# Optimization experiments

Hardware: AMD Instinct MI355X
Metric: run time of the kernel (lower is better)

## Reference

```python
import jax, jax.numpy as jnp
import numpy as np

L = 32      # num_layer
N_ORD = 64  # order_of_a_LTImodel
U = 64      # u_size
Y = 64      # y_size
T = 8192    # sequence length
SCALE = 0.05  # keep block-bidiagonal A spectrally stable over 8192 steps


def setup_inputs() -> dict:
    key = jax.random.key(0)
    k_u, k_a, k_b0, k_bl, k_c = jax.random.split(key, 5)
    inp = {
        "input": jax.random.normal(k_u, (T, U), dtype=jnp.float32),
        # per-layer A_i weights (diagonal blocks)
        "A_stack": jax.random.normal(k_a, (L, N_ORD, N_ORD), dtype=jnp.float32) * SCALE,
        # layer-0 B (maps u -> state)
        "B0": jax.random.normal(k_b0, (N_ORD, U), dtype=jnp.float32) * SCALE,
        # layer i>=1 B weights (sub-diagonal coupling blocks)
        "B_lower": jax.random.normal(k_bl, (L - 1, N_ORD, N_ORD), dtype=jnp.float32) * SCALE,
        # per-layer C_i weights, concatenated along columns in forward
        "C_stack": jax.random.normal(k_c, (L, Y, N_ORD), dtype=jnp.float32),
        # D is frozen zeros (feedthrough=False)
        "D_w": jnp.zeros((Y, U), dtype=jnp.float32),
    }
    return inp


def _assemble(A_stack, B0, B_lower, C_stack):
    l, n, _ = A_stack.shape
    S = l * n
    A = jnp.zeros((S, S), A_stack.dtype)
    for i in range(l):  # fixed small structural loop
        A = A.at[i * n:(i + 1) * n, i * n:(i + 1) * n].set(A_stack[i])
    for i in range(1, l):
        A = A.at[i * n:(i + 1) * n, (i - 1) * n:i * n].set(B_lower[i - 1])
    B = jnp.concatenate([B0, jnp.zeros((S - n, B0.shape[1]), B0.dtype)], axis=0)
    # torch.cat([C_i], dim=1): [Y, L*n]
    C = jnp.transpose(C_stack, (1, 0, 2)).reshape(C_stack.shape[1], S)
    return A, B, C


def reference(input, A_stack, B0, B_lower, C_stack, D_w):
    A, B, C = _assemble(A_stack, B0, B_lower, C_stack)
    S = A.shape[0]
    x0 = jnp.zeros((S,), input.dtype)

    def step(x, u):
        y = C @ x + D_w @ u      # output BEFORE state update (y_t uses x_t)
        x_next = A @ x + B @ u
        return x_next, y

    _, ys = jax.lax.scan(step, x0, input)
    return ys  # [T, Y]
```

## Files before the change

### kernel.cpp

```cpp
#include <hip/hip_runtime.h>


#define LYR 32
#define NO  64
#define TSEQ 8192
#define PAD 32
#define PR2 (TSEQ+PAD)
#define PB2 ((size_t)PR2*NO)
#define KQ  2048

typedef _Float16 h16;
typedef _Float16 h16x8 __attribute__((ext_vector_type(8)));
typedef float    f32x4 __attribute__((ext_vector_type(4)));

#define MFMA16(a,b,c) __builtin_amdgcn_mfma_f32_16x16x32_f16((a),(b),(c),0,0,0)

__global__ __launch_bounds__(256) void prep_build(
    const float* __restrict__ u, const float* __restrict__ B0,
    const float* __restrict__ Bl, const float* __restrict__ Cst,
    const float* __restrict__ Ast,
    h16* __restrict__ xq, h16* __restrict__ ccast,
    h16* __restrict__ SN, h16* __restrict__ ST,
    h16* __restrict__ ktq, float* __restrict__ Dacc)
{
    __shared__ __align__(16) h16   Ah[64*72];
    __shared__ __align__(16) h16   kT[64*72];
    __shared__ __align__(16) float kf[64*68];
    const int tid = threadIdx.x;

    if (blockIdx.x < 32) {
        const int layer = blockIdx.x;
        const bool wantST = (layer & 3) == 0;
        const float* k0 = (layer == 0) ? B0 : (Bl + (size_t)(layer-1)*4096);
        const float* Aw = Ast + (size_t)layer*4096;
        for (int e8 = tid; e8 < 512; e8 += 256) {
            int n = e8 >> 3, m0 = (e8 & 7) << 3;
            f32x4 a0 = *(const f32x4*)&Aw[n*64 + m0];
            f32x4 a1 = *(const f32x4*)&Aw[n*64 + m0 + 4];
            h16 ah[8];
            #pragma unroll
            for (int t = 0; t < 4; t++) { ah[t] = (h16)a0[t]; ah[4+t] = (h16)a1[t]; }
            *(int4*)&Ah[n*72 + m0] = *(int4*)&ah[0];
            f32x4 b0 = *(const f32x4*)&k0[n*64 + m0];
            f32x4 b1 = *(const f32x4*)&k0[n*64 + m0 + 4];
            *(f32x4*)&kf[n*68 + m0]     = b0;
            *(f32x4*)&kf[n*68 + m0 + 4] = b1;
        }
        __syncthreads();

        const int wv = tid >> 6, lane = tid & 63, r = lane & 15, q = lane >> 4;
        const h16x8 a0 = *(const h16x8*)&Ah[(wv*16 + r)*72 + q*8];
        const h16x8 a1 = *(const h16x8*)&Ah[(wv*16 + r)*72 + 32 + q*8];

        for (int j = 0; j < 16; j++) {
            if (j > 0) {
                f32x4 acc[4] = {};
                #pragma unroll
                for (int c = 0; c < 4; c++) {
                    h16x8 b0 = *(const h16x8*)&kT[(c*16 + r)*72 + q*8];
                    h16x8 b1 = *(const h16x8*)&kT[(c*16 + r)*72 + 32 + q*8];
                    acc[c] = MFMA16(a0, b0, acc[c]);
                    acc[c] = MFMA16(a1, b1, acc[c]);
                }
                #pragma unroll
                for (int c = 0; c < 4; c++)
                    #pragma unroll
                    for (int g4 = 0; g4 < 4; g4++)
                        kf[(wv*16 + q*4 + g4)*68 + c*16 + r] = acc[c][g4];
                __syncthreads();
            }
            size_t base = (size_t)(layer*16 + j)*4096;
            for (int e8 = tid; e8 < 512; e8 += 256) {
                int n = e8 >> 3, m0 = (e8 & 7) << 3;
                f32x4 v0 = *(const f32x4*)&kf[n*68 + m0];
                f32x4 v1 = *(const f32x4*)&kf[n*68 + m0 + 4];
                h16 o[8];
                #pragma unroll
                for (int t = 0; t < 4; t++) { o[t] = (h16)v0[t]; o[4+t] = (h16)v1[t]; }
                if (!wantST)
                    *(int4*)&SN[base + (size_t)n*64 + m0] = *(int4*)&o[0];
                #pragma unroll
                for (int t = 0; t < 8; t++)
                    kT[(m0 + t)*72 + n] = o[t];
                if (wantST) {
                    h16 o2[8];
                    #pragma unroll
                    for (int t = 0; t < 8; t++) o2[t] = (h16)kf[(m0 + t)*68 + n];
                    *(int4*)&ST[base + (size_t)n*64 + m0] = *(int4*)&o2[0];
                }
            }
            __syncthreads();
        }
        return;
    }

    const int s1 = 256;
    const int s2 = 65536;
    const int s3 = 1792;
    const int s4 = 16384;
    const int s5 = 131072;
    const int s6 = 262144;
    const int total = s1+s2+s3+s4+s5+s6;
    const int4 z4 = make_int4(0,0,0,0);
    for (int e0 = (blockIdx.x - 32)*256 + tid; e0 < total; e0 += 512*256) {
        int e = e0;
        if (e < s1) { *(int4*)&xq[e*8] = z4; continue; }
        e -= s1;
        if (e < s2) {
            int el = e*8;
            f32x4 f0 = *(const f32x4*)&u[el];
            f32x4 f1 = *(const f32x4*)&u[el+4];
            h16 ov[8];
            #pragma unroll
            for (int j = 0; j < 4; j++) { ov[j] = (h16)f0[j]; ov[4+j] = (h16)f1[j]; }
            *(int4*)&xq[PAD*NO + el] = *(int4*)&ov[0];
            continue;
        }
        e -= s2;
        if (e < s3) {
            int b = e >> 8, off = (e & 255)*8;
            *(int4*)&xq[(size_t)(b+1)*PB2 + off] = z4;
            continue;
        }
        e -= s3;
        if (e < s4) {
            int el = e*8;
            f32x4 f0 = *(const f32x4*)&Cst[el];
            f32x4 f1 = *(const f32x4*)&Cst[el+4];
            h16 ov[8];
            #pragma unroll
            for (int j = 0; j < 4; j++) { ov[j] = (h16)f0[j]; ov[4+j] = (h16)f1[j]; }
            *(int4*)&ccast[el] = *(int4*)&ov[0];
            continue;
        }
        e -= s4;
        if (e < s5) { *(int4*)&ktq[e*8] = z4; continue; }
        e -= s5;
        *(int4*)&Dacc[e*4] = z4;
    }
}

__device__ __forceinline__ void comp_mm(const h16* __restrict__ X,
                                        const h16* __restrict__ Y,
                                        int wv, int r, int q, f32x4 acc[4])
{
    h16x8 a0 = *(const h16x8*)(X + (wv*16 + r)*64 + q*8);
    h16x8 a1 = *(const h16x8*)(X + (wv*16 + r)*64 + 32 + q*8);
    #pragma unroll
    for (int c = 0; c < 4; c++) {
        h16x8 b0 = *(const h16x8*)(Y + (c*16 + r)*64 + q*8);
        h16x8 b1 = *(const h16x8*)(Y + (c*16 + r)*64 + 32 + q*8);
        acc[c] = MFMA16(a0, b0, acc[c]);
        acc[c] = MFMA16(a1, b1, acc[c]);
    }
}

__global__ __launch_bounds__(256) void compose2(
    const h16* __restrict__ SN, const h16* __restrict__ ST,
    const h16* __restrict__ cc, h16* __restrict__ P2T,
    float* __restrict__ Dacc)
{
    const int tid = threadIdx.x, wv = tid>>6, lane = tid&63, r = lane&15, q = lane>>4;
    f32x4 acc[4] = {};
    int bid = blockIdx.x;
    if (bid < 248) {
        int g = bid / 31, m2 = bid % 31;
        int j0 = m2 > 15 ? m2 - 15 : 0;
        int j1 = m2 < 15 ? m2 : 15;
        const h16* X = SN + ((size_t)(4*g+1)*16 + j0)*4096;
        const h16* Y = ST + ((size_t)(4*g)*16 + (m2 - j0))*4096;
        for (int it = 0; it <= j1 - j0; ++it) {
            comp_mm(X, Y, wv, r, q, acc);
            X += 4096; Y -= 4096;
        }
        h16* o = P2T + ((size_t)g*31 + m2)*4096;
        #pragma unroll
        for (int c = 0; c < 4; c++)
            #pragma unroll
            for (int g4 = 0; g4 < 4; g4++)
                o[(c*16+r)*64 + wv*16 + q*4 + g4] = (h16)acc[c][g4];
    } else {
        int idx = bid - 248, g = idx >> 4, j = idx & 15;
        comp_mm(cc + (size_t)(4*g)*4096, ST + ((size_t)(4*g)*16 + j)*4096, wv, r, q, acc);
        float* Dd = Dacc + ((size_t)g*32 + j)*4096;
        #pragma unroll
        for (int c = 0; c < 4; c++)
            #pragma unroll
            for (int g4 = 0; g4 < 4; g4++)
                atomicAdd(&Dd[(wv*16 + q*4 + g4)*64 + c*16 + r], acc[c][g4]);
    }
}

__global__ __launch_bounds__(256) void compose3(
    const h16* __restrict__ SN, const h16* __restrict__ cc,
    const h16* __restrict__ P2T, h16* __restrict__ P3T,
    float* __restrict__ Dacc)
{
    const int tid = threadIdx.x, wv = tid>>6, lane = tid&63, r = lane&15, q = lane>>4;
    f32x4 acc[4] = {};
    int bid = blockIdx.x;
    if (bid < 240) {
        int g = bid / 30, m3 = bid % 30;
        int j1 = m3 < 15 ? m3 : 15;
        const h16* X = SN + ((size_t)(4*g+2)*16)*4096;
        const h16* Y = P2T + ((size_t)g*31 + m3)*4096;
        for (int it = 0; it <= j1; ++it) {
            comp_mm(X, Y, wv, r, q, acc);
            X += 4096; Y -= 4096;
        }
        h16* o = P3T + ((size_t)g*30 + m3)*4096;
        #pragma unroll
        for (int c = 0; c < 4; c++)
            #pragma unroll
            for (int g4 = 0; g4 < 4; g4++)
                o[(c*16+r)*64 + wv*16 + q*4 + g4] = (h16)acc[c][g4];
    } else {
        int idx = bid - 240, g = idx / 31, m2 = idx % 31;
        comp_mm(cc + (size_t)(4*g+1)*4096, P2T + ((size_t)g*31 + m2)*4096, wv, r, q, acc);
        float* Dd = Dacc + ((size_t)g*32 + m2 + 1)*4096;
        #pragma unroll
        for (int c = 0; c < 4; c++)
            #pragma unroll
            for (int g4 = 0; g4 < 4; g4++)
                atomicAdd(&Dd[(wv*16 + q*4 + g4)*64 + c*16 + r], acc[c][g4]);
    }
}

__global__ __launch_bounds__(256) void compose4(
    const h16* __restrict__ SN, const h16* __restrict__ cc,
    const h16* __restrict__ P3T, h16* __restrict__ ktq,
    float* __restrict__ Dacc)
{
    __shared__ h16 ldsT[64*72];
    const int tid = threadIdx.x, wv = tid>>6, lane = tid&63, r = lane&15, q = lane>>4;
    f32x4 acc[4] = {};
    int bid = blockIdx.x;
    if (bid < 232) {
        int g = bid / 29, m4 = bid % 29;
        int j1 = m4 < 15 ? m4 : 15;
        const h16* X = SN + ((size_t)(4*g+3)*16)*4096;
        const h16* Y = P3T + ((size_t)g*30 + m4)*4096;
        for (int it = 0; it <= j1; ++it) {
            comp_mm(X, Y, wv, r, q, acc);
            X += 4096; Y -= 4096;
        }
        h16* kq = ktq + (size_t)g*131072 + (size_t)(28 - m4)*64;
        #pragma unroll
        for (int c = 0; c < 4; c++)
            #pragma unroll
            for (int g4 = 0; g4 < 4; g4++) {
                h16 v = (h16)acc[c][g4];
                kq[(size_t)(wv*16 + q*4 + g4)*KQ + c*16 + r] = v;
                ldsT[(c*16+r)*72 + wv*16 + q*4 + g4] = v;
            }
        __syncthreads();
        f32x4 acc2[4] = {};
        const h16* Xc = cc + (size_t)(4*g+3)*4096;
        h16x8 a0 = *(const h16x8*)(Xc + (wv*16 + r)*64 + q*8);
        h16x8 a1 = *(const h16x8*)(Xc + (wv*16 + r)*64 + 32 + q*8);
        #pragma unroll
        for (int c = 0; c < 4; c++) {
            h16x8 b0 = *(const h16x8*)(&ldsT[(c*16+r)*72 + q*8]);
            h16x8 b1 = *(const h16x8*)(&ldsT[(c*16+r)*72 + 32 + q*8]);
            acc2[c] = MFMA16(a0, b0, acc2[c]);
            acc2[c] = MFMA16(a1, b1, acc2[c]);
        }
        float* Dd = Dacc + ((size_t)g*32 + m4 + 3)*4096;
        #pragma unroll
        for (int c = 0; c < 4; c++)
            #pragma unroll
            for (int g4 = 0; g4 < 4; g4++)
                atomicAdd(&Dd[(wv*16 + q*4 + g4)*64 + c*16 + r], acc2[c][g4]);
    } else {
        int idx = bid - 232, g = idx / 30, m3 = idx % 30;
        comp_mm(cc + (size_t)(4*g+2)*4096, P3T + ((size_t)g*30 + m3)*4096, wv, r, q, acc);
        float* Dd = Dacc + ((size_t)g*32 + m3 + 2)*4096;
        #pragma unroll
        for (int c = 0; c < 4; c++)
            #pragma unroll
            for (int g4 = 0; g4 < 4; g4++)
                atomicAdd(&Dd[(wv*16 + q*4 + g4)*64 + c*16 + r], acc[c][g4]);
    }
}

__global__ __launch_bounds__(256) void castD(const float* __restrict__ Dacc,
                                             h16* __restrict__ ktd)
{
    const int total4 = 8*32*4096/4;
    for (int idx4 = blockIdx.x*256 + threadIdx.x; idx4 < total4; idx4 += 256*256) {
        int idx = idx4 << 2;
        int gdo = idx >> 12;
        int g = gdo >> 5, dd = gdo & 31;
        int rem = idx & 4095;
        int y = rem >> 6, m = rem & 63;
        f32x4 f = *(const f32x4*)&Dacc[idx];
        h16 o4[4];
        #pragma unroll
        for (int t = 0; t < 4; t++) o4[t] = (h16)f[t];
        *(int2*)&ktd[(size_t)g*131072 + (size_t)y*KQ + (31 - dd)*64 + m] = *(int2*)&o4[0];
    }
}

template<int WRST>
__global__ __launch_bounds__(512) void stage(
    const h16* __restrict__ pin, h16* __restrict__ pout,
    const h16* __restrict__ ktqg, const h16* __restrict__ ktdg,
    float* __restrict__ out, int first)
{
    __shared__ __align__(16) h16   win[96*72];
    __shared__ __align__(16) float red[4*32*68];
    const int tid = threadIdx.x;
    const size_t t0 = (size_t)blockIdx.x * 64;

    for (int e = tid; e < 96*8; e += 512) {
        int rr = e >> 3, cc = e & 7;
        *(int4*)&win[rr*72 + cc*8] = *(const int4*)&pin[(t0 + rr)*64 + cc*8];
    }
    __syncthreads();

    const int wv = tid >> 6, lane = tid & 63, r = lane & 15, q = lane >> 4;
    const int half = wv >> 2, kq = wv & 3;
    const bool active = WRST || (half == 1);
    f32x4 acc[2][2][4] = {};
    if (active) {
        const h16* kb = half ? ktdg : ktqg;
        const h16* abase = &win[(r + kq*8)*72 + q*8];
        const h16* bbase = kb + (size_t)r*KQ + kq*512 + q*8;
#define LDA(st, s, ls) (*(const h16x8*)(abase + ((st)*32 + (s)*16 + ((ls)>>1))*72 + ((ls)&1)*32))
#define LDB(c, ls) (*(const h16x8*)(bbase + (size_t)(c)*(16*KQ) + (ls)*32))
        h16x8 a[2][2][2], b[2][4];
        #pragma unroll
        for (int sl = 0; sl < 2; sl++) {
            #pragma unroll
            for (int st = 0; st < 2; st++)
                #pragma unroll
                for (int s = 0; s < 2; s++) a[sl][st][s] = LDA(st, s, sl);
            #pragma unroll
            for (int c = 0; c < 4; c++) b[sl][c] = LDB(c, sl);
        }
        #pragma unroll
        for (int ls = 0; ls < 16; ls++) {
            h16x8 ca[2][2], cb[4];
            #pragma unroll
            for (int st = 0; st < 2; st++)
                #pragma unroll
                for (int s = 0; s < 2; s++) ca[st][s] = a[ls&1][st][s];
            #pragma unroll
            for (int c = 0; c < 4; c++) cb[c] = b[ls&1][c];
            if (ls < 14) {
                #pragma unroll
                for (int st = 0; st < 2; st++)
                    #pragma unroll
                    for (int s = 0; s < 2; s++) a[ls&1][st][s] = LDA(st, s, ls+2);
                #pragma unroll
                for (int c = 0; c < 4; c++) b[ls&1][c] = LDB(c, ls+2);
            }
            #pragma unroll
            for (int st = 0; st < 2; st++)
                #pragma unroll
                for (int s = 0; s < 2; s++)
                    #pragma unroll
                    for (int c = 0; c < 4; c++)
                        acc[st][s][c] = MFMA16(ca[st][s], cb[c], acc[st][s][c]);
        }
#undef LDA
#undef LDB
    }

    const int rh = half * (2*32*68);
    #pragma unroll
    for (int st = 0; st < 2; st++) {
        __syncthreads();
        if (active && kq >= 2) {
            float* myred = red + rh + (kq-2)*(32*68);
            #pragma unroll
            for (int s2 = 0; s2 < 2; s2++)
                #pragma unroll
                for (int c = 0; c < 4; c++)
                    #pragma unroll
                    for (int g4 = 0; g4 < 4; g4++)
                        myred[(s2*16 + q*4 + g4)*68 + c*16 + r] = acc[st][s2][c][g4];
        }
        __syncthreads();
        if (active && kq < 2) {
            float* myred = red + rh + kq*(32*68);
            #pragma unroll
            for (int s2 = 0; s2 < 2; s2++)
                #pragma unroll
                for (int c = 0; c < 4; c++)
                    #pragma unroll
                    for (int g4 = 0; g4 < 4; g4++)
                        myred[(s2*16 + q*4 + g4)*68 + c*16 + r] += acc[st][s2][c][g4];
        }
        __syncthreads();
        if (WRST && tid < 256) {
            int orow = tid >> 3, cb2 = (tid & 7) << 3;
            f32x4 u0 = *(const f32x4*)&red[orow*68 + cb2];
            f32x4 u1 = *(const f32x4*)&red[orow*68 + cb2 + 4];
            f32x4 v0 = *(const f32x4*)&red[32*68 + orow*68 + cb2];
            f32x4 v1 = *(const f32x4*)&red[32*68 + orow*68 + cb2 + 4];
            u0 += v0; u1 += v1;
            h16 ov[8];
            #pragma unroll
            for (int j = 0; j < 4; j++) { ov[j] = (h16)u0[j]; ov[4+j] = (h16)u1[j]; }
            *(int4*)&pout[(PAD + t0 + st*32 + orow)*64 + cb2] = *(int4*)&ov[0];
        }
        if (tid >= 256) {
            int t2 = tid - 256;
            int orow = t2 >> 3, cb2 = (t2 & 7) << 3;
            const float* base = red + 2*32*68;
            f32x4 u0 = *(const f32x4*)&base[orow*68 + cb2];
            f32x4 u1 = *(const f32x4*)&base[orow*68 + cb2 + 4];
            f32x4 v0 = *(const f32x4*)&base[32*68 + orow*68 + cb2];
            f32x4 v1 = *(const f32x4*)&base[32*68 + orow*68 + cb2 + 4];
            u0 += v0; u1 += v1;
            float* op = out + (t0 + st*32 + orow)*64 + cb2;
            if (first) {
                *(f32x4*)op = u0; *(f32x4*)(op+4) = u1;
            } else {
                f32x4 o0 = *(f32x4*)op, o1 = *(f32x4*)(op+4);
                o0 += u0; o1 += u1;
                *(f32x4*)op = o0; *(f32x4*)(op+4) = o1;
            }
        }
    }
}

extern "C" void kernel_launch(void* const* d_in, const int* in_sizes, int n_in,
                              void* d_out, int out_size, void* d_ws, size_t ws_size,
                              hipStream_t stream)
{
    const float* u   = (const float*)d_in[0];
    const float* Ast = (const float*)d_in[1];
    const float* B0  = (const float*)d_in[2];
    const float* Bl  = (const float*)d_in[3];
    const float* Cst = (const float*)d_in[4];
    float* out = (float*)d_out;
    (void)in_sizes; (void)n_in; (void)out_size; (void)ws_size;

    char* ws = (char*)d_ws;
    h16*   xq    = (h16*)ws;
    h16*   ccast = (h16*)(ws + 8421376);
    h16*   SN    = (h16*)(ws + 8683520);
    h16*   ST    = (h16*)(ws + 12877824);
    h16*   P2T   = (h16*)(ws + 17072128);
    h16*   P3T   = (h16*)(ws + 19103744);
    h16*   ktq   = (h16*)(ws + 21069824);
    h16*   ktd   = (h16*)(ws + 23166976);
    float* Dacc  = (float*)(ws + 25264128);

    prep_build<<<544, 256, 0, stream>>>(u, B0, Bl, Cst, Ast, xq, ccast, SN, ST, ktq, Dacc);
    compose2<<<376, 256, 0, stream>>>(SN, ST, ccast, P2T, Dacc);
    compose3<<<488, 256, 0, stream>>>(SN, ccast, P2T, P3T, Dacc);
    compose4<<<472, 256, 0, stream>>>(SN, ccast, P3T, ktq, Dacc);
    castD<<<256, 256, 0, stream>>>(Dacc, ktd);
    for (int g = 0; g < 7; g++) {
        stage<1><<<TSEQ/64, 512, 0, stream>>>(xq + (size_t)g*PB2, xq + (size_t)(g+1)*PB2,
                                              ktq + (size_t)g*131072, ktd + (size_t)g*131072,
                                              out, g == 0);
    }
    stage<0><<<TSEQ/64, 512, 0, stream>>>(xq + (size_t)7*PB2, xq,
                                          ktq + (size_t)7*131072, ktd + (size_t)7*131072,
                                          out, 0);
}
```

Measured before the change: 303.0 us.

## Replace grouped state-passing stages with tree-composed full impulse response and single GEMM

The previous approach composed per-group kernels and then ran eight sequential stage launches that propagated intermediate states through the sequence. The new code builds the full Markov-parameter kernel (C·A^k·B for all relevant lags) through a binary-tree composition over layers, in six level kernels. It then computes the output directly as one convolution-like GEMM of the input against that kernel, with a 3072-wide reduction. This removes the serial stage chain and its intermediate state traffic and atomics, but adds more composition passes and larger fp32/fp16 workspace buffers.

```diff
diff --git a/kernel.cpp b/kernel.cpp
--- a/kernel.cpp
+++ b/kernel.cpp
@@ -1,13 +1,11 @@
 #include <hip/hip_runtime.h>
 
 
-#define LYR 32
-#define NO  64
+#define NO   64
 #define TSEQ 8192
-#define PAD 32
-#define PR2 (TSEQ+PAD)
-#define PB2 ((size_t)PR2*NO)
-#define KQ  2048
+#define PADU 48
+#define UR   (TSEQ+PADU)
+#define KY   3072
 
 typedef _Float16 h16;
 typedef _Float16 h16x8 __attribute__((ext_vector_type(8)));
@@ -19,9 +17,8 @@
     const float* __restrict__ u, const float* __restrict__ B0,
     const float* __restrict__ Bl, const float* __restrict__ Cst,
     const float* __restrict__ Ast,
-    h16* __restrict__ xq, h16* __restrict__ ccast,
-    h16* __restrict__ SN, h16* __restrict__ ST,
-    h16* __restrict__ ktq, float* __restrict__ Dacc)
+    h16* __restrict__ uq, h16* __restrict__ ccast,
+    h16* __restrict__ TN, h16* __restrict__ TT)
 {
     __shared__ __align__(16) h16   Ah[64*72];
     __shared__ __align__(16) h16   kT[64*72];
@@ -30,7 +27,6 @@
 
     if (blockIdx.x < 32) {
         const int layer = blockIdx.x;
-        const bool wantST = (layer & 3) == 0;
         const float* k0 = (layer == 0) ? B0 : (Bl + (size_t)(layer-1)*4096);
         const float* Aw = Ast + (size_t)layer*4096;
         for (int e8 = tid; e8 < 512; e8 += 256) {
@@ -41,10 +37,8 @@
             #pragma unroll
             for (int t = 0; t < 4; t++) { ah[t] = (h16)a0[t]; ah[4+t] = (h16)a1[t]; }
             *(int4*)&Ah[n*72 + m0] = *(int4*)&ah[0];
-            f32x4 b0 = *(const f32x4*)&k0[n*64 + m0];
-            f32x4 b1 = *(const f32x4*)&k0[n*64 + m0 + 4];
-            *(f32x4*)&kf[n*68 + m0]     = b0;
-            *(f32x4*)&kf[n*68 + m0 + 4] = b1;
+            *(f32x4*)&kf[n*68 + m0]     = *(const f32x4*)&k0[n*64 + m0];
+            *(f32x4*)&kf[n*68 + m0 + 4] = *(const f32x4*)&k0[n*64 + m0 + 4];
         }
         __syncthreads();
 
@@ -77,34 +71,28 @@
                 h16 o[8];
                 #pragma unroll
                 for (int t = 0; t < 4; t++) { o[t] = (h16)v0[t]; o[4+t] = (h16)v1[t]; }
-                if (!wantST)
-                    *(int4*)&SN[base + (size_t)n*64 + m0] = *(int4*)&o[0];
+                *(int4*)&TN[base + (size_t)n*64 + m0] = *(int4*)&o[0];
                 #pragma unroll
                 for (int t = 0; t < 8; t++)
                     kT[(m0 + t)*72 + n] = o[t];
-                if (wantST) {
-                    h16 o2[8];
-                    #pragma unroll
-                    for (int t = 0; t < 8; t++) o2[t] = (h16)kf[(m0 + t)*68 + n];
-                    *(int4*)&ST[base + (size_t)n*64 + m0] = *(int4*)&o2[0];
-                }
+                h16 o2[8];
+                #pragma unroll
+                for (int t = 0; t < 8; t++) o2[t] = (h16)kf[(m0 + t)*68 + n];
+                *(int4*)&TT[base + (size_t)n*64 + m0] = *(int4*)&o2[0];
             }
             __syncthreads();
         }
         return;
     }
 
-    const int s1 = 256;
+    const int s1 = 384;
     const int s2 = 65536;
-    const int s3 = 1792;
-    const int s4 = 16384;
-    const int s5 = 131072;
-    const int s6 = 262144;
-    const int total = s1+s2+s3+s4+s5+s6;
+    const int s3 = 16384;
+    const int total = s1 + s2 + s3;
     const int4 z4 = make_int4(0,0,0,0);
     for (int e0 = (blockIdx.x - 32)*256 + tid; e0 < total; e0 += 512*256) {
         int e = e0;
-        if (e < s1) { *(int4*)&xq[e*8] = z4; continue; }
+        if (e < s1) { *(int4*)&uq[e*8] = z4; continue; }
         e -= s1;
         if (e < s2) {
             int el = e*8;
@@ -113,30 +101,17 @@
             h16 ov[8];
             #pragma unroll
             for (int j = 0; j < 4; j++) { ov[j] = (h16)f0[j]; ov[4+j] = (h16)f1[j]; }
-            *(int4*)&xq[PAD*NO + el] = *(int4*)&ov[0];
+            *(int4*)&uq[PADU*NO + el] = *(int4*)&ov[0];
             continue;
         }
         e -= s2;
-        if (e < s3) {
-            int b = e >> 8, off = (e & 255)*8;
-            *(int4*)&xq[(size_t)(b+1)*PB2 + off] = z4;
-            continue;
-        }
-        e -= s3;
-        if (e < s4) {
-            int el = e*8;
-            f32x4 f0 = *(const f32x4*)&Cst[el];
-            f32x4 f1 = *(const f32x4*)&Cst[el+4];
-            h16 ov[8];
-            #pragma unroll
-            for (int j = 0; j < 4; j++) { ov[j] = (h16)f0[j]; ov[4+j] = (h16)f1[j]; }
-            *(int4*)&ccast[el] = *(int4*)&ov[0];
-            continue;
-        }
-        e -= s4;
-        if (e < s5) { *(int4*)&ktq[e*8] = z4; continue; }
-        e -= s5;
-        *(int4*)&Dacc[e*4] = z4;
+        int el = e*8;
+        f32x4 f0 = *(const f32x4*)&Cst[el];
+        f32x4 f1 = *(const f32x4*)&Cst[el+4];
+        h16 ov[8];
+        #pragma unroll
+        for (int j = 0; j < 4; j++) { ov[j] = (h16)f0[j]; ov[4+j] = (h16)f1[j]; }
+        *(int4*)&ccast[el] = *(int4*)&ov[0];
     }
 }
 
@@ -155,274 +130,285 @@
     }
 }
 
-__global__ __launch_bounds__(256) void compose2(
-    const h16* __restrict__ SN, const h16* __restrict__ ST,
-    const h16* __restrict__ cc, h16* __restrict__ P2T,
-    float* __restrict__ Dacc)
+__device__ __forceinline__ void conv_loop(const h16* X, const h16* Y, int n,
+                                          int wv, int r, int q, f32x4 acc[4])
+{
+    for (int it = 0; it < n; ++it) {
+        comp_mm(X, Y, wv, r, q, acc);
+        X += 4096; Y -= 4096;
+    }
+}
+__device__ __forceinline__ void add_copy(const float* __restrict__ DF,
+                                         int wv, int r, int q, f32x4 acc[4])
+{
+    #pragma unroll
+    for (int c = 0; c < 4; c++)
+        #pragma unroll
+        for (int g4 = 0; g4 < 4; g4++)
+            acc[c][g4] += DF[(size_t)(wv*16 + q*4 + g4)*64 + c*16 + r];
+}
+__device__ __forceinline__ void write_N(h16* o, int wv, int r, int q, const f32x4 acc[4])
+{
+    #pragma unroll
+    for (int c = 0; c < 4; c++)
+        #pragma unroll
+        for (int g4 = 0; g4 < 4; g4++)
+            o[(size_t)(wv*16 + q*4 + g4)*64 + c*16 + r] = (h16)acc[c][g4];
+}
+__device__ __forceinline__ void write_T(h16* o, int wv, int r, int q, const f32x4 acc[4])
+{
+    #pragma unroll
+    for (int c = 0; c < 4; c++)
+        #pragma unroll
+        for (int g4 = 0; g4 < 4; g4++)
+            o[(size_t)(c*16 + r)*64 + wv*16 + q*4 + g4] = (h16)acc[c][g4];
+}
+__device__ __forceinline__ void write_F(float* o, int wv, int r, int q, const f32x4 acc[4])
+{
+    #pragma unroll
+    for (int c = 0; c < 4; c++)
+        #pragma unroll
+        for (int g4 = 0; g4 < 4; g4++)
+            o[(size_t)(wv*16 + q*4 + g4)*64 + c*16 + r] = acc[c][g4];
+}
+#define IMAX(a,b) ((a)>(b)?(a):(b))
+#define IMIN(a,b) ((a)<(b)?(a):(b))
+
+__global__ __launch_bounds__(256) void lvl1(
+    const h16* __restrict__ TN, const h16* __restrict__ TT,
+    const h16* __restrict__ cc,
+    h16* __restrict__ P2N, h16* __restrict__ P2T,
+    h16* __restrict__ DSN, float* __restrict__ DSF)
 {
     const int tid = threadIdx.x, wv = tid>>6, lane = tid&63, r = lane&15, q = lane>>4;
     f32x4 acc[4] = {};
     int bid = blockIdx.x;
-    if (bid < 248) {
-        int g = bid / 31, m2 = bid % 31;
-        int j0 = m2 > 15 ? m2 - 15 : 0;
-        int j1 = m2 < 15 ? m2 : 15;
-        const h16* X = SN + ((size_t)(4*g+1)*16 + j0)*4096;
-        const h16* Y = ST + ((size_t)(4*g)*16 + (m2 - j0))*4096;
-        for (int it = 0; it <= j1 - j0; ++it) {
-            comp_mm(X, Y, wv, r, q, acc);
-            X += 4096; Y -= 4096;
-        }
-        h16* o = P2T + ((size_t)g*31 + m2)*4096;
-        #pragma unroll
-        for (int c = 0; c < 4; c++)
-            #pragma unroll
-            for (int g4 = 0; g4 < 4; g4++)
-                o[(c*16+r)*64 + wv*16 + q*4 + g4] = (h16)acc[c][g4];
+    if (bid < 496) {
+        int p = bid / 31, m = bid % 31, D = m + 2;
+        int j0 = IMAX(1, D-16), j1 = IMIN(16, D-1);
+        conv_loop(TN + ((size_t)((2*p+1)*16 + j0-1))*4096,
+                  TT + ((size_t)((2*p)*16 + D-j0-1))*4096, j1-j0+1, wv, r, q, acc);
+        write_N(P2N + ((size_t)(p*31 + m))*4096, wv, r, q, acc);
+        write_T(P2T + ((size_t)(p*31 + m))*4096, wv, r, q, acc);
     } else {
-        int idx = bid - 248, g = idx >> 4, j = idx & 15;
-        comp_mm(cc + (size_t)(4*g)*4096, ST + ((size_t)(4*g)*16 + j)*4096, wv, r, q, acc);
-        float* Dd = Dacc + ((size_t)g*32 + j)*4096;
-        #pragma unroll
-        for (int c = 0; c < 4; c++)
-            #pragma unroll
-            for (int g4 = 0; g4 < 4; g4++)
-                atomicAdd(&Dd[(wv*16 + q*4 + g4)*64 + c*16 + r], acc[c][g4]);
-    }
-}
-
-__global__ __launch_bounds__(256) void compose3(
-    const h16* __restrict__ SN, const h16* __restrict__ cc,
-    const h16* __restrict__ P2T, h16* __restrict__ P3T,
-    float* __restrict__ Dacc)
+        int idx = bid - 496, l = idx >> 4, j = idx & 15;
+        conv_loop(cc + (size_t)l*4096, TT + ((size_t)(l*16 + j))*4096, 1, wv, r, q, acc);
+        write_N(DSN + ((size_t)(l*16 + j))*4096, wv, r, q, acc);
+        write_F(DSF + ((size_t)(l*16 + j))*4096, wv, r, q, acc);
+    }
+}
+
+__global__ __launch_bounds__(256) void lvl2(
+    const h16* __restrict__ DSN, const float* __restrict__ DSF,
+    const h16* __restrict__ TT,
+    const h16* __restrict__ P2N, const h16* __restrict__ P2T,
+    h16* __restrict__ D2N, float* __restrict__ D2F,
+    h16* __restrict__ P4N, h16* __restrict__ P4T)
 {
     const int tid = threadIdx.x, wv = tid>>6, lane = tid&63, r = lane&15, q = lane>>4;
     f32x4 acc[4] = {};
     int bid = blockIdx.x;
-    if (bid < 240) {
-        int g = bid / 30, m3 = bid % 30;
-        int j1 = m3 < 15 ? m3 : 15;
-        const h16* X = SN + ((size_t)(4*g+2)*16)*4096;
-        const h16* Y = P2T + ((size_t)g*31 + m3)*4096;
-        for (int it = 0; it <= j1; ++it) {
-            comp_mm(X, Y, wv, r, q, acc);
-            X += 4096; Y -= 4096;
-        }
-        h16* o = P3T + ((size_t)g*30 + m3)*4096;
-        #pragma unroll
-        for (int c = 0; c < 4; c++)
-            #pragma unroll
-            for (int g4 = 0; g4 < 4; g4++)
-                o[(c*16+r)*64 + wv*16 + q*4 + g4] = (h16)acc[c][g4];
+    if (bid < 512) {
+        int p = bid >> 5, m = bid & 31, D = m + 1;
+        int j0 = IMAX(1, D-16), j1 = IMIN(16, D-1);
+        if (j1 >= j0)
+            conv_loop(DSN + ((size_t)((2*p+1)*16 + j0-1))*4096,
+                      TT + ((size_t)((2*p)*16 + D-j0-1))*4096, j1-j0+1, wv, r, q, acc);
+        if (D <= 16) add_copy(DSF + ((size_t)((2*p)*16 + D-1))*4096, wv, r, q, acc);
+        write_N(D2N + ((size_t)(p*32 + m))*4096, wv, r, q, acc);
+        write_F(D2F + ((size_t)(p*32 + m))*4096, wv, r, q, acc);
     } else {
-        int idx = bid - 240, g = idx / 31, m2 = idx % 31;
-        comp_mm(cc + (size_t)(4*g+1)*4096, P2T + ((size_t)g*31 + m2)*4096, wv, r, q, acc);
-        float* Dd = Dacc + ((size_t)g*32 + m2 + 1)*4096;
-        #pragma unroll
-        for (int c = 0; c < 4; c++)
-            #pragma unroll
-            for (int g4 = 0; g4 < 4; g4++)
-                atomicAdd(&Dd[(wv*16 + q*4 + g4)*64 + c*16 + r], acc[c][g4]);
-    }
-}
-
-__global__ __launch_bounds__(256) void compose4(
-    const h16* __restrict__ SN, const h16* __restrict__ cc,
-    const h16* __restrict__ P3T, h16* __restrict__ ktq,
-    float* __restrict__ Dacc)
-{
-    __shared__ h16 ldsT[64*72];
+        int idx = bid - 512, qd = idx >> 5, m = idx & 31, D = m + 4;
+        int j0 = IMAX(2, D-32), j1 = IMIN(32, D-2);
+        conv_loop(P2N + ((size_t)((2*qd+1)*31 + j0-2))*4096,
+                  P2T + ((size_t)((2*qd)*31 + D-j0-2))*4096, j1-j0+1, wv, r, q, acc);
+        write_N(P4N + ((size_t)(qd*32 + m))*4096, wv, r, q, acc);
+        write_T(P4T + ((size_t)(qd*32 + m))*4096, wv, r, q, acc);
+    }
+}
+
+__global__ __launch_bounds__(256) void lvl3(
+    const h16* __restrict__ D2N, const float* __restrict__ D2F,
+    const h16* __restrict__ P2T,
+    const h16* __restrict__ P4N, const h16* __restrict__ P4T,
+    h16* __restrict__ D4N, float* __restrict__ D4F,
+    h16* __restrict__ P8N, h16* __restrict__ P8T)
+{
     const int tid = threadIdx.x, wv = tid>>6, lane = tid&63, r = lane&15, q = lane>>4;
     f32x4 acc[4] = {};
     int bid = blockIdx.x;
-    if (bid < 232) {
-        int g = bid / 29, m4 = bid % 29;
-        int j1 = m4 < 15 ? m4 : 15;
-        const h16* X = SN + ((size_t)(4*g+3)*16)*4096;
-        const h16* Y = P3T + ((size_t)g*30 + m4)*4096;
-        for (int it = 0; it <= j1; ++it) {
-            comp_mm(X, Y, wv, r, q, acc);
-            X += 4096; Y -= 4096;
-        }
-        h16* kq = ktq + (size_t)g*131072 + (size_t)(28 - m4)*64;
-        #pragma unroll
-        for (int c = 0; c < 4; c++)
-            #pragma unroll
-            for (int g4 = 0; g4 < 4; g4++) {
-                h16 v = (h16)acc[c][g4];
-                kq[(size_t)(wv*16 + q*4 + g4)*KQ + c*16 + r] = v;
-                ldsT[(c*16+r)*72 + wv*16 + q*4 + g4] = v;
-            }
-        __syncthreads();
-        f32x4 acc2[4] = {};
-        const h16* Xc = cc + (size_t)(4*g+3)*4096;
-        h16x8 a0 = *(const h16x8*)(Xc + (wv*16 + r)*64 + q*8);
-        h16x8 a1 = *(const h16x8*)(Xc + (wv*16 + r)*64 + 32 + q*8);
-        #pragma unroll
-        for (int c = 0; c < 4; c++) {
-            h16x8 b0 = *(const h16x8*)(&ldsT[(c*16+r)*72 + q*8]);
-            h16x8 b1 = *(const h16x8*)(&ldsT[(c*16+r)*72 + 32 + q*8]);
-            acc2[c] = MFMA16(a0, b0, acc2[c]);
-            acc2[c] = MFMA16(a1, b1, acc2[c]);
-        }
-        float* Dd = Dacc + ((size_t)g*32 + m4 + 3)*4096;
-        #pragma unroll
-        for (int c = 0; c < 4; c++)
-            #pragma unroll
-            for (int g4 = 0; g4 < 4; g4++)
-                atomicAdd(&Dd[(wv*16 + q*4 + g4)*64 + c*16 + r], acc2[c][g4]);
+    if (bid < 384) {
+        int qd = bid / 48, m = bid % 48, D = m + 1;
+        int j0 = IMAX(1, D-32), j1 = IMIN(32, D-2);
+        if (j1 >= j0)
+            conv_loop(D2N + ((size_t)((2*qd+1)*32 + j0-1))*4096,
+                      P2T + ((size_t)((2*qd)*31 + D-j0-2))*4096, j1-j0+1, wv, r, q, acc);
+        if (D <= 32) add_copy(D2F + ((size_t)((2*qd)*32 + D-1))*4096, wv, r, q, acc);
+        write_N(D4N + ((size_t)(qd*48 + m))*4096, wv, r, q, acc);
+        write_F(D4F + ((size_t)(qd*48 + m))*4096, wv, r, q, acc);
     } else {
-        int idx = bid - 232, g = idx / 30, m3 = idx % 30;
-        comp_mm(cc + (size_t)(4*g+2)*4096, P3T + ((size_t)g*30 + m3)*4096, wv, r, q, acc);
-        float* Dd = Dacc + ((size_t)g*32 + m3 + 2)*4096;
-        #pragma unroll
-        for (int c = 0; c < 4; c++)
-            #pragma unroll
-            for (int g4 = 0; g4 < 4; g4++)
-                atomicAdd(&Dd[(wv*16 + q*4 + g4)*64 + c*16 + r], acc[c][g4]);
-    }
-}
-
-__global__ __launch_bounds__(256) void castD(const float* __restrict__ Dacc,
-                                             h16* __restrict__ ktd)
-{
-    const int total4 = 8*32*4096/4;
-    for (int idx4 = blockIdx.x*256 + threadIdx.x; idx4 < total4; idx4 += 256*256) {
-        int idx = idx4 << 2;
-        int gdo = idx >> 12;
-        int g = gdo >> 5, dd = gdo & 31;
-        int rem = idx & 4095;
-        int y = rem >> 6, m = rem & 63;
-        f32x4 f = *(const f32x4*)&Dacc[idx];
-        h16 o4[4];
-        #pragma unroll
-        for (int t = 0; t < 4; t++) o4[t] = (h16)f[t];
-        *(int2*)&ktd[(size_t)g*131072 + (size_t)y*KQ + (31 - dd)*64 + m] = *(int2*)&o4[0];
-    }
-}
-
-template<int WRST>
-__global__ __launch_bounds__(512) void stage(
-    const h16* __restrict__ pin, h16* __restrict__ pout,
-    const h16* __restrict__ ktqg, const h16* __restrict__ ktdg,
-    float* __restrict__ out, int first)
-{
-    __shared__ __align__(16) h16   win[96*72];
+        int idx = bid - 384, o = idx >> 5, m = idx & 31, D = m + 8;
+        int j0 = IMAX(4, D-35), j1 = IMIN(35, D-4);
+        conv_loop(P4N + ((size_t)((2*o+1)*32 + j0-4))*4096,
+                  P4T + ((size_t)((2*o)*32 + D-j0-4))*4096, j1-j0+1, wv, r, q, acc);
+        write_N(P8N + ((size_t)(o*32 + m))*4096, wv, r, q, acc);
+        write_T(P8T + ((size_t)(o*32 + m))*4096, wv, r, q, acc);
+    }
+}
+
+__global__ __launch_bounds__(256) void lvl4(
+    const h16* __restrict__ D4N, const float* __restrict__ D4F,
+    const h16* __restrict__ P4T,
+    const h16* __restrict__ P8N, const h16* __restrict__ P8T,
+    h16* __restrict__ D8N, float* __restrict__ D8F,
+    h16* __restrict__ P16T)
+{
+    const int tid = threadIdx.x, wv = tid>>6, lane = tid&63, r = lane&15, q = lane>>4;
+    f32x4 acc[4] = {};
+    int bid = blockIdx.x;
+    if (bid < 192) {
+        int o = bid / 48, m = bid % 48, D = m + 1;
+        int j0 = IMAX(1, D-35), j1 = IMIN(48, D-4);
+        if (j1 >= j0)
+            conv_loop(D4N + ((size_t)((2*o+1)*48 + j0-1))*4096,
+                      P4T + ((size_t)((2*o)*32 + D-j0-4))*4096, j1-j0+1, wv, r, q, acc);
+        add_copy(D4F + ((size_t)((2*o)*48 + D-1))*4096, wv, r, q, acc);
+        write_N(D8N + ((size_t)(o*48 + m))*4096, wv, r, q, acc);
+        write_F(D8F + ((size_t)(o*48 + m))*4096, wv, r, q, acc);
+    } else {
+        int m = bid - 192, D = m + 16;
+        int j0 = IMAX(8, D-39), j1 = IMIN(39, D-8);
+        conv_loop(P8N + ((size_t)(32 + j0-8))*4096,
+                  P8T + ((size_t)(D-j0-8))*4096, j1-j0+1, wv, r, q, acc);
+        write_T(P16T + (size_t)m*4096, wv, r, q, acc);
+    }
+}
+
+__global__ __launch_bounds__(256) void lvl5(
+    const h16* __restrict__ D8N, const float* __restrict__ D8F,
+    const h16* __restrict__ P8T,
+    h16* __restrict__ D16N, float* __restrict__ D16F)
+{
+    const int tid = threadIdx.x, wv = tid>>6, lane = tid&63, r = lane&15, q = lane>>4;
+    f32x4 acc[4] = {};
+    int h = blockIdx.x / 48, m = blockIdx.x % 48, D = m + 1;
+    int j0 = IMAX(1, D-39), j1 = IMIN(48, D-8);
+    if (j1 >= j0)
+        conv_loop(D8N + ((size_t)((2*h+1)*48 + j0-1))*4096,
+                  P8T + ((size_t)((2*h)*32 + D-j0-8))*4096, j1-j0+1, wv, r, q, acc);
+    add_copy(D8F + ((size_t)((2*h)*48 + D-1))*4096, wv, r, q, acc);
+    write_N(D16N + ((size_t)(h*48 + m))*4096, wv, r, q, acc);
+    write_F(D16F + ((size_t)(h*48 + m))*4096, wv, r, q, acc);
+}
+
+__global__ __launch_bounds__(256) void lvl6(
+    const h16* __restrict__ D16N, const float* __restrict__ D16F,
+    const h16* __restrict__ P16T, h16* __restrict__ ktd)
+{
+    const int tid = threadIdx.x, wv = tid>>6, lane = tid&63, r = lane&15, q = lane>>4;
+    f32x4 acc[4] = {};
+    int m = blockIdx.x, D = m + 1;
+    int j0 = IMAX(1, D-47), j1 = IMIN(48, D-16);
+    if (j1 >= j0)
+        conv_loop(D16N + ((size_t)(48 + j0-1))*4096,
+                  P16T + ((size_t)(D-j0-16))*4096, j1-j0+1, wv, r, q, acc);
+    add_copy(D16F + (size_t)m*4096, wv, r, q, acc);
+    #pragma unroll
+    for (int c = 0; c < 4; c++)
+        #pragma unroll
+        for (int g4 = 0; g4 < 4; g4++) {
+            int y = wv*16 + q*4 + g4;
+            ktd[(size_t)y*KY + (size_t)(48-D)*64 + c*16 + r] = (h16)acc[c][g4];
+        }
+}
+
+__global__ __launch_bounds__(512) void ygemm(
+    const h16* __restrict__ uq, const h16* __restrict__ ktd,
+    float* __restrict__ out)
+{
+    __shared__ __align__(16) h16   win[80*72];
     __shared__ __align__(16) float red[4*32*68];
     const int tid = threadIdx.x;
-    const size_t t0 = (size_t)blockIdx.x * 64;
-
-    for (int e = tid; e < 96*8; e += 512) {
+    const size_t t0 = (size_t)blockIdx.x * 32;
+
+    for (int e = tid; e < 80*8; e += 512) {
         int rr = e >> 3, cc = e & 7;
-        *(int4*)&win[rr*72 + cc*8] = *(const int4*)&pin[(t0 + rr)*64 + cc*8];
+        *(int4*)&win[rr*72 + cc*8] = *(const int4*)&uq[(t0 + rr)*64 + cc*8];
     }
     __syncthreads();
 
     const int wv = tid >> 6, lane = tid & 63, r = lane & 15, q = lane >> 4;
-    const int half = wv >> 2, kq = wv & 3;
-    const bool active = WRST || (half == 1);
-    f32x4 acc[2][2][4] = {};
-    if (active) {
-        const h16* kb = half ? ktdg : ktqg;
-        const h16* abase = &win[(r + kq*8)*72 + q*8];
-        const h16* bbase = kb + (size_t)r*KQ + kq*512 + q*8;
-#define LDA(st, s, ls) (*(const h16x8*)(abase + ((st)*32 + (s)*16 + ((ls)>>1))*72 + ((ls)&1)*32))
-#define LDB(c, ls) (*(const h16x8*)(bbase + (size_t)(c)*(16*KQ) + (ls)*32))
-        h16x8 a[2][2][2], b[2][4];
-        #pragma unroll
-        for (int sl = 0; sl < 2; sl++) {
-            #pragma unroll
-            for (int st = 0; st < 2; st++)
-                #pragma unroll
-                for (int s = 0; s < 2; s++) a[sl][st][s] = LDA(st, s, sl);
-            #pragma unroll
-            for (int c = 0; c < 4; c++) b[sl][c] = LDB(c, sl);
-        }
-        #pragma unroll
-        for (int ls = 0; ls < 16; ls++) {
-            h16x8 ca[2][2], cb[4];
-            #pragma unroll
-            for (int st = 0; st < 2; st++)
-                #pragma unroll
-                for (int s = 0; s < 2; s++) ca[st][s] = a[ls&1][st][s];
-            #pragma unroll
-            for (int c = 0; c < 4; c++) cb[c] = b[ls&1][c];
-            if (ls < 14) {
-                #pragma unroll
-                for (int st = 0; st < 2; st++)
-                    #pragma unroll
-                    for (int s = 0; s < 2; s++) a[ls&1][st][s] = LDA(st, s, ls+2);
-                #pragma unroll
-                for (int c = 0; c < 4; c++) b[ls&1][c] = LDB(c, ls+2);
-            }
-            #pragma unroll
-            for (int st = 0; st < 2; st++)
-                #pragma unroll
-                for (int s = 0; s < 2; s++)
-                    #pragma unroll
-                    for (int c = 0; c < 4; c++)
-                        acc[st][s][c] = MFMA16(ca[st][s], cb[c], acc[st][s][c]);
-        }
+    const h16* abase = &win[(r + wv*6)*72 + q*8];
+    const h16* bbase = ktd + (size_t)r*KY + wv*384 + q*8;
+#define LDA(s, ls) (*(const h16x8*)(abase + ((s)*16 + ((ls)>>1))*72 + ((ls)&1)*32))
+#define LDB(c, ls) (*(const h16x8*)(bbase + (size_t)(c)*(16*KY) + (ls)*32))
+    f32x4 acc[2][4] = {};
+    h16x8 a[2][2], b[2][4];
+    #pragma unroll
+    for (int sl = 0; sl < 2; sl++) {
+        #pragma unroll
+        for (int s = 0; s < 2; s++) a[sl][s] = LDA(s, sl);
+        #pragma unroll
+        for (int c = 0; c < 4; c++) b[sl][c] = LDB(c, sl);
+    }
+    #pragma unroll
+    for (int ls = 0; ls < 12; ls++) {
+        h16x8 ca[2], cb[4];
+        #pragma unroll
+        for (int s = 0; s < 2; s++) ca[s] = a[ls&1][s];
+        #pragma unroll
+        for (int c = 0; c < 4; c++) cb[c] = b[ls&1][c];
+        if (ls < 10) {
+            #pragma unroll
+            for (int s = 0; s < 2; s++) a[ls&1][s] = LDA(s, ls+2);
+            #pragma unroll
+            for (int c = 0; c < 4; c++) b[ls&1][c] = LDB(c, ls+2);
+        }
+        #pragma unroll
+        for (int s = 0; s < 2; s++)
+            #pragma unroll
+            for (int c = 0; c < 4; c++)
+                acc[s][c] = MFMA16(ca[s], cb[c], acc[s][c]);
+    }
 #undef LDA
 #undef LDB
-    }
-
-    const int rh = half * (2*32*68);
-    #pragma unroll
-    for (int st = 0; st < 2; st++) {
-        __syncthreads();
-        if (active && kq >= 2) {
-            float* myred = red + rh + (kq-2)*(32*68);
-            #pragma unroll
-            for (int s2 = 0; s2 < 2; s2++)
-                #pragma unroll
-                for (int c = 0; c < 4; c++)
-                    #pragma unroll
-                    for (int g4 = 0; g4 < 4; g4++)
-                        myred[(s2*16 + q*4 + g4)*68 + c*16 + r] = acc[st][s2][c][g4];
-        }
-        __syncthreads();
-        if (active && kq < 2) {
-            float* myred = red + rh + kq*(32*68);
-            #pragma unroll
-            for (int s2 = 0; s2 < 2; s2++)
-                #pragma unroll
-                for (int c = 0; c < 4; c++)
-                    #pragma unroll
-                    for (int g4 = 0; g4 < 4; g4++)
-                        myred[(s2*16 + q*4 + g4)*68 + c*16 + r] += acc[st][s2][c][g4];
-        }
-        __syncthreads();
-        if (WRST && tid < 256) {
-            int orow = tid >> 3, cb2 = (tid & 7) << 3;
-            f32x4 u0 = *(const f32x4*)&red[orow*68 + cb2];
-            f32x4 u1 = *(const f32x4*)&red[orow*68 + cb2 + 4];
-            f32x4 v0 = *(const f32x4*)&red[32*68 + orow*68 + cb2];
-            f32x4 v1 = *(const f32x4*)&red[32*68 + orow*68 + cb2 + 4];
-            u0 += v0; u1 += v1;
-            h16 ov[8];
-            #pragma unroll
-            for (int j = 0; j < 4; j++) { ov[j] = (h16)u0[j]; ov[4+j] = (h16)u1[j]; }
-            *(int4*)&pout[(PAD + t0 + st*32 + orow)*64 + cb2] = *(int4*)&ov[0];
-        }
-        if (tid >= 256) {
-            int t2 = tid - 256;
-            int orow = t2 >> 3, cb2 = (t2 & 7) << 3;
-            const float* base = red + 2*32*68;
-            f32x4 u0 = *(const f32x4*)&base[orow*68 + cb2];
-            f32x4 u1 = *(const f32x4*)&base[orow*68 + cb2 + 4];
-            f32x4 v0 = *(const f32x4*)&base[32*68 + orow*68 + cb2];
-            f32x4 v1 = *(const f32x4*)&base[32*68 + orow*68 + cb2 + 4];
-            u0 += v0; u1 += v1;
-            float* op = out + (t0 + st*32 + orow)*64 + cb2;
-            if (first) {
-                *(f32x4*)op = u0; *(f32x4*)(op+4) = u1;
-            } else {
-                f32x4 o0 = *(f32x4*)op, o1 = *(f32x4*)(op+4);
-                o0 += u0; o1 += u1;
-                *(f32x4*)op = o0; *(f32x4*)(op+4) = o1;
-            }
-        }
+    const int kq = wv & 3;
+    const int rh = (wv >> 2) * (2*32*68);
+    __syncthreads();
+    if (kq >= 2) {
+        float* myred = red + rh + (kq-2)*(32*68);
+        #pragma unroll
+        for (int s2 = 0; s2 < 2; s2++)
+            #pragma unroll
+            for (int c = 0; c < 4; c++)
+                #pragma unroll
+                for (int g4 = 0; g4 < 4; g4++)
+                    myred[(s2*16 + q*4 + g4)*68 + c*16 + r] = acc[s2][c][g4];
+    }
+    __syncthreads();
+    if (kq < 2) {
+        float* myred = red + rh + kq*(32*68);
+        #pragma unroll
+        for (int s2 = 0; s2 < 2; s2++)
+            #pragma unroll
+            for (int c = 0; c < 4; c++)
+                #pragma unroll
+                for (int g4 = 0; g4 < 4; g4++)
+                    myred[(s2*16 + q*4 + g4)*68 + c*16 + r] += acc[s2][c][g4];
+    }
+    __syncthreads();
+    if (tid < 256) {
+        int orow = tid >> 3, cb2 = (tid & 7) << 3;
+        f32x4 u0 = *(const f32x4*)&red[orow*68 + cb2];
+        f32x4 u1 = *(const f32x4*)&red[orow*68 + cb2 + 4];
+        #pragma unroll
+        for (int bnk = 1; bnk < 4; bnk++) {
+            u0 += *(const f32x4*)&red[bnk*(32*68) + orow*68 + cb2];
+            u1 += *(const f32x4*)&red[bnk*(32*68) + orow*68 + cb2 + 4];
+        }
+        size_t obase = (t0 + orow)*64 + cb2;
+        *(f32x4*)&out[obase]     = u0;
+        *(f32x4*)&out[obase + 4] = u1;
     }
 }
 
@@ -439,27 +425,35 @@
     (void)in_sizes; (void)n_in; (void)out_size; (void)ws_size;
 
     char* ws = (char*)d_ws;
-    h16*   xq    = (h16*)ws;
-    h16*   ccast = (h16*)(ws + 8421376);
-    h16*   SN    = (h16*)(ws + 8683520);
-    h16*   ST    = (h16*)(ws + 12877824);
-    h16*   P2T   = (h16*)(ws + 17072128);
-    h16*   P3T   = (h16*)(ws + 19103744);
-    h16*   ktq   = (h16*)(ws + 21069824);
-    h16*   ktd   = (h16*)(ws + 23166976);
-    float* Dacc  = (float*)(ws + 25264128);
-
-    prep_build<<<544, 256, 0, stream>>>(u, B0, Bl, Cst, Ast, xq, ccast, SN, ST, ktq, Dacc);
-    compose2<<<376, 256, 0, stream>>>(SN, ST, ccast, P2T, Dacc);
-    compose3<<<488, 256, 0, stream>>>(SN, ccast, P2T, P3T, Dacc);
-    compose4<<<472, 256, 0, stream>>>(SN, ccast, P3T, ktq, Dacc);
-    castD<<<256, 256, 0, stream>>>(Dacc, ktd);
-    for (int g = 0; g < 7; g++) {
-        stage<1><<<TSEQ/64, 512, 0, stream>>>(xq + (size_t)g*PB2, xq + (size_t)(g+1)*PB2,
-                                              ktq + (size_t)g*131072, ktd + (size_t)g*131072,
-                                              out, g == 0);
-    }
-    stage<0><<<TSEQ/64, 512, 0, stream>>>(xq + (size_t)7*PB2, xq,
-                                          ktq + (size_t)7*131072, ktd + (size_t)7*131072,
-                                          out, 0);
-}
+    h16*   uq    = (h16*)  (ws + 0);
+    h16*   ccast = (h16*)  (ws + 1054720);
+    h16*   TN    = (h16*)  (ws + 1316864);
+    h16*   TT    = (h16*)  (ws + 5511168);
+    h16*   P2N   = (h16*)  (ws + 9705472);
+    h16*   P2T   = (h16*)  (ws + 13768704);
+    h16*   P4N   = (h16*)  (ws + 17831936);
+    h16*   P4T   = (h16*)  (ws + 19929088);
+    h16*   P8N   = (h16*)  (ws + 22026240);
+    h16*   P8T   = (h16*)  (ws + 23074816);
+    h16*   P16T  = (h16*)  (ws + 24123392);
+    h16*   DSN   = (h16*)  (ws + 24385536);
+    float* DSF   = (float*)(ws + 28579840);
+    h16*   D2N   = (h16*)  (ws + 36968448);
+    float* D2F   = (float*)(ws + 41162752);
+    h16*   D4N   = (h16*)  (ws + 49551360);
+    float* D4F   = (float*)(ws + 52697088);
+    h16*   D8N   = (h16*)  (ws + 58988544);
+    float* D8F   = (float*)(ws + 60561408);
+    h16*   D16N  = (h16*)  (ws + 63707136);
+    float* D16F  = (float*)(ws + 64493568);
+    h16*   ktd   = (h16*)  (ws + 66066432);
+
+    prep_build<<<544, 256, 0, stream>>>(u, B0, Bl, Cst, Ast, uq, ccast, TN, TT);
+    lvl1<<<1008, 256, 0, stream>>>(TN, TT, ccast, P2N, P2T, DSN, DSF);
+    lvl2<<<768, 256, 0, stream>>>(DSN, DSF, TT, P2N, P2T, D2N, D2F, P4N, P4T);
+    lvl3<<<512, 256, 0, stream>>>(D2N, D2F, P2T, P4N, P4T, D4N, D4F, P8N, P8T);
+    lvl4<<<224, 256, 0, stream>>>(D4N, D4F, P4T, P8N, P8T, D8N, D8F, P16T);
+    lvl5<<<96, 256, 0, stream>>>(D8N, D8F, P8T, D16N, D16F);
+    lvl6<<<48, 256, 0, stream>>>(D16N, D16F, P16T, ktd);
+    ygemm<<<TSEQ/32, 512, 0, stream>>>(uq, ktd, out);
+}
```

Measured after the change: 367.6 us. 21.3% more time.
